# Performance work log

Measured on AMD Instinct MI355X. Metric: run time of the kernel, lower is better.

## Reference

```python
import jax, jax.numpy as jnp
import numpy as np

TOPK_FRAC = 0.9
LEAKY_SLOPE = 0.01
BN_EPS = 1e-5


def setup_inputs() -> dict:
    key = jax.random.key(0)
    k1, k2 = jax.random.split(key)
    B, C_in, N, C_out = 8, 256, 2048, 256
    x = jax.random.normal(k1, (B, C_in, N), dtype=jnp.float32)
    stdv = 1.0 / np.sqrt(C_out)
    weight = jax.random.uniform(k2, (C_in, C_out), dtype=jnp.float32, minval=-stdv, maxval=stdv)
    bn_weight = jnp.zeros((C_out,), dtype=jnp.float32)
    bn_bias = jnp.zeros((C_out,), dtype=jnp.float32)
    return {"x": x, "weight": weight, "bn_weight": bn_weight, "bn_bias": bn_bias}


def _norm_adj(xn):
    # xn: [B, N, C]
    adj = jax.nn.softmax(jnp.einsum('bnc,bmc->bnm', xn, xn), axis=-1)  # [B,N,N]
    N = adj.shape[1]
    k = int(round(N * TOPK_FRAC))
    topv, _ = jax.lax.top_k(adj, k)                     # [B,N,k]
    thresh = topv[..., -1:]                              # k-th largest per row
    return jnp.where(adj >= thresh, adj, 0.0)           # keep top-k, zero rest


def reference(x, weight, bn_weight, bn_bias):
    # x: [B, C_in, N] -> [B, N, C_in]
    xn = jnp.transpose(x, (0, 2, 1))
    adj = _norm_adj(xn)                                  # [B,N,N]
    support = jnp.einsum('bnc,cd->bnd', xn, weight)      # [B,N,C_out]
    out = jnp.einsum('bnm,bmd->bnd', adj, support)       # [B,N,C_out]
    out = jnp.transpose(out, (0, 2, 1))                  # [B,C_out,N]
    out = jnp.where(out >= 0, out, LEAKY_SLOPE * out)    # LeakyReLU
    # BatchNorm1d (training-mode batch stats) over (B, N) per channel
    mean = jnp.mean(out, axis=(0, 2), keepdims=True)
    var = jnp.mean(jnp.square(out - mean), axis=(0, 2), keepdims=True)
    out = (out - mean) * jax.lax.rsqrt(var + BN_EPS)
    return out * bn_weight[None, :, None] + bn_bias[None, :, None]
```

## Files before the change

kernel.cpp:

```cpp
#include <hip/hip_runtime.h>

#define B_ 8
#define C_ 256
#define N_ 2048
#define D_ 256
#define KKEEP 1843
#define LEAKY 0.01f
#define EPS 1e-5f

using short8  = __attribute__((ext_vector_type(8))) short;
using ushort8 = __attribute__((ext_vector_type(8))) unsigned short;
using ushort4v = __attribute__((ext_vector_type(4))) unsigned short;
using f32x4   = __attribute__((ext_vector_type(4))) float;

__device__ inline unsigned short f2bf(float x) {
  unsigned u = __float_as_uint(x);
  u += 0x7fffu + ((u >> 16) & 1u);
  return (unsigned short)(u >> 16);
}
__device__ inline float bf2f(unsigned short u) { return __uint_as_float(((unsigned)u) << 16); }

__device__ inline void gload16(const void* g, void* l) {
  __builtin_amdgcn_global_load_lds(
      (const __attribute__((address_space(1))) void*)g,
      (__attribute__((address_space(3))) void*)l, 16, 0, 0);
}

__global__ __launch_bounds__(256) void k_transpose_cast(const float* __restrict__ src,
                                                        unsigned short* __restrict__ dst,
                                                        int rows, int cols,
                                                        size_t srcBatch, size_t dstBatch) {
  __shared__ float tile[32][33];
  int b = blockIdx.z;
  src += (size_t)b * srcBatch;
  dst += (size_t)b * dstBatch;
  int i0 = blockIdx.y * 32;
  int j0 = blockIdx.x * 32;
  int t = threadIdx.x;
  int tc = t & 31, tr = t >> 5;
#pragma unroll
  for (int k = 0; k < 4; ++k)
    tile[tr + k * 8][tc] = src[(size_t)(i0 + tr + k * 8) * cols + j0 + tc];
  __syncthreads();
  int r2 = t >> 3, q = t & 7;
  ushort4v v;
#pragma unroll
  for (int l = 0; l < 4; ++l) v[l] = f2bf(tile[q * 4 + l][r2]);
  *(ushort4v*)&dst[(size_t)(j0 + r2) * rows + i0 + q * 4] = v;
}

template<int K_, int NX>
__global__ __launch_bounds__(256) void k_gemm(const short* __restrict__ A,
                                              const short* __restrict__ Bt,
                                              unsigned short* __restrict__ Cout,
                                              size_t aStride, size_t bStride, size_t cStride,
                                              int ldc) {
  __shared__ short As[128][64];
  __shared__ short Bs[128][64];
  int lin = blockIdx.x;
  int b = lin & 7;
  int rest = lin >> 3;
  int bxi = rest % NX, byi = rest / NX;
  const short* Ab = A + (size_t)b * aStride;
  const short* Bb = Bt + (size_t)b * bStride;
  int bi = byi * 128, bj = bxi * 128;
  int t = threadIdx.x, lane = t & 63, wid = t >> 6;
  int wr = (wid >> 1) * 64, wc = (wid & 1) * 64;
  int fr = lane & 15;
  int wbase = wid * 512;

  f32x4 acc[4][4];
  f32x4 z = {0.f, 0.f, 0.f, 0.f};
#pragma unroll
  for (int i = 0; i < 4; ++i)
#pragma unroll
    for (int j = 0; j < 4; ++j) acc[i][j] = z;

  for (int c0 = 0; c0 < K_; c0 += 64) {
    if (c0) __syncthreads();
#pragma unroll
    for (int i = 0; i < 4; ++i) {
      int li = i * 256 + t;
      int row = li >> 3, ch = li & 7;
      int sw = ((ch ^ (row & 7)) << 3);
      gload16(Ab + (size_t)(bi + row) * K_ + c0 + sw, (short*)As + i * 2048 + wbase);
      gload16(Bb + (size_t)(bj + row) * K_ + c0 + sw, (short*)Bs + i * 2048 + wbase);
    }
    __syncthreads();
#pragma unroll
    for (int ksub = 0; ksub < 2; ++ksub) {
      int cA = ksub * 4 + (lane >> 4);
      short8 af[4], bf[4];
#pragma unroll
      for (int f = 0; f < 4; ++f) {
        int R = wr + f * 16 + fr;
        af[f] = *(const short8*)&As[R][(cA ^ (R & 7)) << 3];
        int Rb = wc + f * 16 + fr;
        bf[f] = *(const short8*)&Bs[Rb][(cA ^ (Rb & 7)) << 3];
      }
#pragma unroll
      for (int fi = 0; fi < 4; ++fi)
#pragma unroll
        for (int fj = 0; fj < 4; ++fj)
          acc[fi][fj] = __builtin_amdgcn_mfma_f32_16x16x32_bf16(af[fi], bf[fj], acc[fi][fj], 0, 0, 0);
    }
  }

  int orow = (lane >> 4) * 4;
  int ocol = lane & 15;
#pragma unroll
  for (int fi = 0; fi < 4; ++fi)
#pragma unroll
    for (int fj = 0; fj < 4; ++fj)
#pragma unroll
      for (int r = 0; r < 4; ++r) {
        size_t idx = (size_t)b * cStride +
                     (size_t)(bi + wr + fi * 16 + orow + r) * ldc +
                     (size_t)(bj + wc + fj * 16 + ocol);
        Cout[idx] = f2bf(acc[fi][fj][r]);
      }
}

__global__ __launch_bounds__(256) void k_softmax_topk(unsigned short* __restrict__ S) {
  int t = threadIdx.x;
  int lane = t & 63, wv = t >> 6;
  size_t row = (size_t)blockIdx.x * 4 + wv;
  unsigned short* sr = S + row * N_;

  float e[32];
#pragma unroll
  for (int i = 0; i < 4; ++i) {
    ushort8 raw = *(const ushort8*)(sr + ((size_t)(i * 64 + lane)) * 8);
#pragma unroll
    for (int j = 0; j < 8; ++j) e[i * 8 + j] = bf2f(raw[j]);
  }

  float lm = e[0];
#pragma unroll
  for (int j = 1; j < 32; ++j) lm = fmaxf(lm, e[j]);
#pragma unroll
  for (int m = 1; m <= 16; m <<= 1) lm = fmaxf(lm, __shfl_xor(lm, m));
  lm = fmaxf(__shfl(lm, 0), __shfl(lm, 32));

  float ls = 0.f;
#pragma unroll
  for (int j = 0; j < 32; ++j) { e[j] = __expf(e[j] - lm); ls += e[j]; }
#pragma unroll
  for (int m = 1; m <= 16; m <<= 1) ls += __shfl_xor(ls, m);
  ls = __shfl(ls, 0) + __shfl(ls, 32);
  float inv = 1.0f / ls;

  unsigned kp[16], vo[16];
#pragma unroll
  for (int q = 0; q < 16; ++q)
    kp[q] = (unsigned)f2bf(e[q]) | ((unsigned)f2bf(e[q + 16]) << 16);
#pragma unroll
  for (int q = 0; q < 16; ++q)
    vo[q] = (unsigned)f2bf(e[2 * q] * inv) | ((unsigned)f2bf(e[2 * q + 1] * inv) << 16);

  unsigned tp[16];
#pragma unroll
  for (int q = 0; q < 16; ++q) tp[q] = kp[q];
#pragma unroll
  for (int sI = 0; sI < 4; ++sI) {
    const int s = 8 >> sI;
    const unsigned msk = (s == 8) ? 0x00FF00FFu : (s == 4) ? 0x0F0F0F0Fu
                       : (s == 2) ? 0x33333333u : 0x55555555u;
#pragma unroll
    for (int k = 0; k < 16; ++k) {
      if ((k & s) == 0) {
        unsigned tt = ((tp[k] >> s) ^ tp[k + s]) & msk;
        tp[k + s] ^= tt;
        tp[k]     ^= tt << s;
      }
    }
  }

  unsigned alive = 0xFFFFFFFFu, prefix = 0u;
  int need = KKEEP;
#pragma unroll
  for (int b = 12; b >= 0; b -= 2) {
    unsigned p1 = tp[b + 1], p0 = tp[b];
    unsigned hi = alive & p1;
    unsigned m3 = hi & p0, m2 = hi & ~p0, m1v = (alive & ~p1) & p0;
    unsigned packed = (unsigned)__popc(m3) | ((unsigned)__popc(m2) << 11) |
                      ((unsigned)__popc(m1v) << 22);
#pragma unroll
    for (int m = 1; m <= 16; m <<= 1) packed += __shfl_xor(packed, m);
    unsigned v0 = __shfl(packed, 0), v32 = __shfl(packed, 32);
    int C3 = (int)((v0 & 0x7FFu) + (v32 & 0x7FFu));
    int C2 = (int)(((v0 >> 11) & 0x7FFu) + ((v32 >> 11) & 0x7FFu));
    int C1 = (int)(((v0 >> 22) & 0x7FFu) + ((v32 >> 22) & 0x7FFu));
    int cum2 = C3 + C2, cum1 = cum2 + C1;
    if (C3 >= need)        { alive = m3;  prefix |= 3u << b; }
    else if (cum2 >= need) { alive = m2;  prefix |= 2u << b; need -= C3; }
    else if (cum1 >= need) { alive = m1v; prefix |= 1u << b; need -= cum2; }
    else                   { alive ^= (m3 | m2 | m1v);       need -= cum1; }
  }

#pragma unroll
  for (int i = 0; i < 4; ++i) {
    ushort8 o;
#pragma unroll
    for (int j = 0; j < 8; ++j) {
      int idx = i * 8 + j;
      unsigned key = (kp[idx & 15] >> ((idx >> 4) * 16)) & 0xFFFFu;
      unsigned val = (vo[idx >> 1] >> ((idx & 1) * 16)) & 0xFFFFu;
      o[j] = (key >= prefix) ? (unsigned short)val : (unsigned short)0;
    }
    *(ushort8*)(sr + ((size_t)(i * 64 + lane)) * 8) = o;
  }
}

__global__ __launch_bounds__(256) void k_pv(const short* __restrict__ A,
                                            const short* __restrict__ Bt,
                                            unsigned short* __restrict__ pre,
                                            float* __restrict__ ps, float* __restrict__ pss) {
  __shared__ short As[128][64];
  __shared__ short Bs[64][64];
  int lin = blockIdx.x;
  int b = lin & 7;
  int rest = lin >> 3;
  int bxi = rest & 3;
  int byi = rest >> 2;
  const short* Ab = A + (size_t)b * N_ * N_;
  const short* Bb = Bt + (size_t)b * D_ * N_;
  int bi = byi * 128, bj = bxi * 64;
  int t = threadIdx.x, lane = t & 63, wid = t >> 6;
  int wr = wid * 32;
  int fr = lane & 15;
  int wbase = wid * 512;

  f32x4 acc[2][4];
  f32x4 z = {0.f, 0.f, 0.f, 0.f};
#pragma unroll
  for (int i = 0; i < 2; ++i)
#pragma unroll
    for (int j = 0; j < 4; ++j) acc[i][j] = z;

  for (int c0 = 0; c0 < N_; c0 += 64) {
    if (c0) __syncthreads();
#pragma unroll
    for (int i = 0; i < 4; ++i) {
      int li = i * 256 + t;
      int row = li >> 3, ch = li & 7;
      int sw = ((ch ^ (row & 7)) << 3);
      gload16(Ab + (size_t)(bi + row) * N_ + c0 + sw, (short*)As + i * 2048 + wbase);
      if (i < 2)
        gload16(Bb + (size_t)(bj + row) * N_ + c0 + sw, (short*)Bs + i * 2048 + wbase);
    }
    __syncthreads();
#pragma unroll
    for (int ksub = 0; ksub < 2; ++ksub) {
      int cA = ksub * 4 + (lane >> 4);
      short8 af[2], bf[4];
#pragma unroll
      for (int f = 0; f < 2; ++f) {
        int R = wr + f * 16 + fr;
        af[f] = *(const short8*)&As[R][(cA ^ (R & 7)) << 3];
      }
#pragma unroll
      for (int f = 0; f < 4; ++f) {
        int Rb = f * 16 + fr;
        bf[f] = *(const short8*)&Bs[Rb][(cA ^ (Rb & 7)) << 3];
      }
#pragma unroll
      for (int fi = 0; fi < 2; ++fi)
#pragma unroll
        for (int fj = 0; fj < 4; ++fj)
          acc[fi][fj] = __builtin_amdgcn_mfma_f32_16x16x32_bf16(af[fi], bf[fj], acc[fi][fj], 0, 0, 0);
    }
  }

  int orow = (lane >> 4) * 4;
  int ocol = lane & 15;
  float s4[4] = {0.f, 0.f, 0.f, 0.f}, ss4[4] = {0.f, 0.f, 0.f, 0.f};
#pragma unroll
  for (int fi = 0; fi < 2; ++fi)
#pragma unroll
    for (int rr = 0; rr < 4; ++rr) {
      int rowg = bi + wr + fi * 16 + orow + rr;
      size_t base = ((size_t)b * N_ + rowg) * D_ + bj;
#pragma unroll
      for (int fj = 0; fj < 4; ++fj) {
        float v = acc[fi][fj][rr];
        v = (v >= 0.f) ? v : LEAKY * v;
        pre[base + fj * 16 + ocol] = f2bf(v);
        s4[fj] += v;
        ss4[fj] = fmaf(v, v, ss4[fj]);
      }
    }
#pragma unroll
  for (int fj = 0; fj < 4; ++fj) {
    s4[fj] += __shfl_xor(s4[fj], 16);  s4[fj] += __shfl_xor(s4[fj], 32);
    ss4[fj] += __shfl_xor(ss4[fj], 16); ss4[fj] += __shfl_xor(ss4[fj], 32);
  }
  __syncthreads();
  float* sred = (float*)As;
  if (lane < 16) {
#pragma unroll
    for (int fj = 0; fj < 4; ++fj) {
      sred[(wid * 4 + fj) * 16 + lane] = s4[fj];
      sred[256 + (wid * 4 + fj) * 16 + lane] = ss4[fj];
    }
  }
  __syncthreads();
  if (t < 64) {
    float s = 0.f, ss = 0.f;
#pragma unroll
    for (int w4 = 0; w4 < 4; ++w4) {
      s  += sred[(w4 * 4 + (t >> 4)) * 16 + (t & 15)];
      ss += sred[256 + (w4 * 4 + (t >> 4)) * 16 + (t & 15)];
    }
    ps[(size_t)lin * 64 + t] = s;
    pss[(size_t)lin * 64 + t] = ss;
  }
}

__global__ void k_final(const float* __restrict__ ps, const float* __restrict__ pss,
                        const float* __restrict__ bnw, const float* __restrict__ bnb,
                        float* __restrict__ scale, float* __restrict__ shift) {
  int t = threadIdx.x;
  int bxi = t >> 6, col = t & 63;
  float s = 0.f, ss = 0.f;
  for (int byi = 0; byi < 16; ++byi)
    for (int bb = 0; bb < 8; ++bb) {
      int lin = (byi * 4 + bxi) * 8 + bb;
      s += ps[(size_t)lin * 64 + col];
      ss += pss[(size_t)lin * 64 + col];
    }
  const float invN = 1.0f / (B_ * N_);
  float mean = s * invN;
  float var = fmaf(-mean, mean, ss * invN);
  float istd = rsqrtf(var + EPS);
  float sc = istd * bnw[t];
  scale[t] = sc;
  shift[t] = fmaf(-mean, sc, bnb[t]);
}

__global__ __launch_bounds__(256) void k_out(const unsigned short* __restrict__ pre,
                                             const float* __restrict__ scale,
                                             const float* __restrict__ shift,
                                             float* __restrict__ out) {
  __shared__ float tile[32][33];
  int blk = blockIdx.x;
  int d0 = (blk % (D_ / 32)) * 32;
  int n0 = ((blk / (D_ / 32)) % (N_ / 32)) * 32;
  int b = blk / ((D_ / 32) * (N_ / 32));
  int tc = threadIdx.x & 31;
  int tr = threadIdx.x >> 5;
  const unsigned short* pb = pre + ((size_t)b * N_ + n0) * D_ + d0;
#pragma unroll
  for (int i = 0; i < 4; ++i) {
    int r = tr + i * 8;
    tile[r][tc] = bf2f(pb[(size_t)r * D_ + tc]);
  }
  __syncthreads();
  float* ob = out + ((size_t)b * D_ + d0) * N_ + n0;
#pragma unroll
  for (int i = 0; i < 4; ++i) {
    int r = tr + i * 8;
    float vv = tile[tc][r];
    ob[(size_t)r * N_ + tc] = fmaf(vv, scale[d0 + r], shift[d0 + r]);
  }
}

extern "C" void kernel_launch(void* const* d_in, const int* in_sizes, int n_in,
                              void* d_out, int out_size, void* d_ws, size_t ws_size,
                              hipStream_t stream) {
  const float* x = (const float*)d_in[0];
  const float* W = (const float*)d_in[1];
  const float* bnw = (const float*)d_in[2];
  const float* bnb = (const float*)d_in[3];
  float* out = (float*)d_out;

  char* w = (char*)d_ws;
  short* xt = (short*)w;            w += (size_t)B_ * N_ * C_ * 2;
  short* wt = (short*)w;            w += (size_t)D_ * C_ * 2;
  short* supT = (short*)w;          w += (size_t)B_ * D_ * N_ * 2;
  short* S = (short*)w;             w += (size_t)B_ * N_ * N_ * 2;
  unsigned short* pre = (unsigned short*)w; w += (size_t)B_ * N_ * D_ * 2;
  float* ps = (float*)w;            w += (size_t)512 * 64 * 4;
  float* pss = (float*)w;           w += (size_t)512 * 64 * 4;
  float* scale = (float*)w;         w += D_ * 4;
  float* shift = (float*)w;         w += D_ * 4;

  k_transpose_cast<<<dim3(N_ / 32, C_ / 32, B_), 256, 0, stream>>>(
      x, (unsigned short*)xt, C_, N_, (size_t)C_ * N_, (size_t)N_ * C_);
  k_transpose_cast<<<dim3(D_ / 32, C_ / 32, 1), 256, 0, stream>>>(
      W, (unsigned short*)wt, C_, D_, 0, 0);

  k_gemm<C_, 16><<<dim3(8 * 16 * 2, 1, 1), 256, 0, stream>>>(
      wt, xt, (unsigned short*)supT, 0, (size_t)N_ * C_, (size_t)D_ * N_, N_);

  k_gemm<C_, 16><<<dim3(8 * 16 * 16, 1, 1), 256, 0, stream>>>(
      xt, xt, (unsigned short*)S, (size_t)N_ * C_, (size_t)N_ * C_, (size_t)N_ * N_, N_);

  k_softmax_topk<<<B_ * N_ / 4, 256, 0, stream>>>((unsigned short*)S);

  k_pv<<<dim3(4 * 16 * 8, 1, 1), 256, 0, stream>>>(S, supT, pre, ps, pss);

  k_final<<<1, 256, 0, stream>>>(ps, pss, bnw, bnb, scale, shift);
  k_out<<<B_ * (N_ / 32) * (D_ / 32), 256, 0, stream>>>(pre, scale, shift, out);
}
```

Measured before the change: 108.4 us.

## Interleave batches across blocks for XCD locality and split PV tile over 8 waves

Block indices in transpose, softmax-topk and output kernels are remapped so the batch index is the low bits. This likely keeps each batch's data on one XCD's L2 on the MI355X. The PV GEMM now runs 512 threads with a 4x2 wave grid, each wave computing 32x32 instead of 32x64, to raise wave-level parallelism per tile. The final BN reduction is split across 4 blocks. The trade-off is that each wave does fewer MFMAs per LDS load and the block uses more registers.

```diff
diff --git a/kernel.cpp b/kernel.cpp
--- a/kernel.cpp
+++ b/kernel.cpp
@@ -26,16 +26,24 @@
       (__attribute__((address_space(3))) void*)l, 16, 0, 0);
 }
 
+template<bool PIN>
 __global__ __launch_bounds__(256) void k_transpose_cast(const float* __restrict__ src,
                                                         unsigned short* __restrict__ dst,
-                                                        int rows, int cols,
+                                                        int rows, int cols, int njt,
                                                         size_t srcBatch, size_t dstBatch) {
   __shared__ float tile[32][33];
-  int b = blockIdx.z;
+  int b, i0, j0;
+  if constexpr (PIN) {
+    int lin = blockIdx.x;
+    b = lin & 7;
+    int rest = lin >> 3;
+    j0 = (rest % njt) * 32;
+    i0 = (rest / njt) * 32;
+  } else {
+    b = blockIdx.z; j0 = blockIdx.x * 32; i0 = blockIdx.y * 32;
+  }
   src += (size_t)b * srcBatch;
   dst += (size_t)b * dstBatch;
-  int i0 = blockIdx.y * 32;
-  int j0 = blockIdx.x * 32;
   int t = threadIdx.x;
   int tc = t & 31, tr = t >> 5;
 #pragma unroll
@@ -124,7 +132,10 @@
 __global__ __launch_bounds__(256) void k_softmax_topk(unsigned short* __restrict__ S) {
   int t = threadIdx.x;
   int lane = t & 63, wv = t >> 6;
-  size_t row = (size_t)blockIdx.x * 4 + wv;
+  int lin = blockIdx.x;
+  int b = lin & 7;
+  int grp = lin >> 3;
+  size_t row = (size_t)b * N_ + grp * 4 + wv;
   unsigned short* sr = S + row * N_;
 
   float e[32];
@@ -179,8 +190,8 @@
   unsigned alive = 0xFFFFFFFFu, prefix = 0u;
   int need = KKEEP;
 #pragma unroll
-  for (int b = 12; b >= 0; b -= 2) {
-    unsigned p1 = tp[b + 1], p0 = tp[b];
+  for (int b2 = 12; b2 >= 0; b2 -= 2) {
+    unsigned p1 = tp[b2 + 1], p0 = tp[b2];
     unsigned hi = alive & p1;
     unsigned m3 = hi & p0, m2 = hi & ~p0, m1v = (alive & ~p1) & p0;
     unsigned packed = (unsigned)__popc(m3) | ((unsigned)__popc(m2) << 11) |
@@ -192,10 +203,10 @@
     int C2 = (int)(((v0 >> 11) & 0x7FFu) + ((v32 >> 11) & 0x7FFu));
     int C1 = (int)(((v0 >> 22) & 0x7FFu) + ((v32 >> 22) & 0x7FFu));
     int cum2 = C3 + C2, cum1 = cum2 + C1;
-    if (C3 >= need)        { alive = m3;  prefix |= 3u << b; }
-    else if (cum2 >= need) { alive = m2;  prefix |= 2u << b; need -= C3; }
-    else if (cum1 >= need) { alive = m1v; prefix |= 1u << b; need -= cum2; }
-    else                   { alive ^= (m3 | m2 | m1v);       need -= cum1; }
+    if (C3 >= need)        { alive = m3;  prefix |= 3u << b2; }
+    else if (cum2 >= need) { alive = m2;  prefix |= 2u << b2; need -= C3; }
+    else if (cum1 >= need) { alive = m1v; prefix |= 1u << b2; need -= cum2; }
+    else                   { alive ^= (m3 | m2 | m1v);        need -= cum1; }
   }
 
 #pragma unroll
@@ -212,7 +223,7 @@
   }
 }
 
-__global__ __launch_bounds__(256) void k_pv(const short* __restrict__ A,
+__global__ __launch_bounds__(512) void k_pv(const short* __restrict__ A,
                                             const short* __restrict__ Bt,
                                             unsigned short* __restrict__ pre,
                                             float* __restrict__ ps, float* __restrict__ pss) {
@@ -226,55 +237,52 @@
   const short* Ab = A + (size_t)b * N_ * N_;
   const short* Bb = Bt + (size_t)b * D_ * N_;
   int bi = byi * 128, bj = bxi * 64;
-  int t = threadIdx.x, lane = t & 63, wid = t >> 6;
-  int wr = wid * 32;
+  int t = threadIdx.x, lane = t & 63, w = t >> 6;
+  int wr = (w >> 1) * 32, wc = (w & 1) * 32;
   int fr = lane & 15;
-  int wbase = wid * 512;
-
-  f32x4 acc[2][4];
+
+  f32x4 acc[2][2];
   f32x4 z = {0.f, 0.f, 0.f, 0.f};
 #pragma unroll
   for (int i = 0; i < 2; ++i)
 #pragma unroll
-    for (int j = 0; j < 4; ++j) acc[i][j] = z;
+    for (int j = 0; j < 2; ++j) acc[i][j] = z;
 
   for (int c0 = 0; c0 < N_; c0 += 64) {
     if (c0) __syncthreads();
-#pragma unroll
-    for (int i = 0; i < 4; ++i) {
-      int li = i * 256 + t;
-      int row = li >> 3, ch = li & 7;
+    {
+      int row = t >> 3, ch = t & 7;
       int sw = ((ch ^ (row & 7)) << 3);
-      gload16(Ab + (size_t)(bi + row) * N_ + c0 + sw, (short*)As + i * 2048 + wbase);
-      if (i < 2)
-        gload16(Bb + (size_t)(bj + row) * N_ + c0 + sw, (short*)Bs + i * 2048 + wbase);
+      gload16(Ab + (size_t)(bi + row) * N_ + c0 + sw, (short*)As + w * 512);
+      gload16(Bb + (size_t)(bj + row) * N_ + c0 + sw, (short*)Bs + w * 512);
+      int li = 512 + t;
+      int row1 = li >> 3, ch1 = li & 7;
+      int sw1 = ((ch1 ^ (row1 & 7)) << 3);
+      gload16(Ab + (size_t)(bi + row1) * N_ + c0 + sw1, (short*)As + 4096 + w * 512);
     }
     __syncthreads();
 #pragma unroll
     for (int ksub = 0; ksub < 2; ++ksub) {
       int cA = ksub * 4 + (lane >> 4);
-      short8 af[2], bf[4];
+      short8 af[2], bf[2];
 #pragma unroll
       for (int f = 0; f < 2; ++f) {
         int R = wr + f * 16 + fr;
         af[f] = *(const short8*)&As[R][(cA ^ (R & 7)) << 3];
-      }
-#pragma unroll
-      for (int f = 0; f < 4; ++f) {
-        int Rb = f * 16 + fr;
+        int Rb = wc + f * 16 + fr;
         bf[f] = *(const short8*)&Bs[Rb][(cA ^ (Rb & 7)) << 3];
       }
 #pragma unroll
       for (int fi = 0; fi < 2; ++fi)
 #pragma unroll
-        for (int fj = 0; fj < 4; ++fj)
+        for (int fj = 0; fj < 2; ++fj)
           acc[fi][fj] = __builtin_amdgcn_mfma_f32_16x16x32_bf16(af[fi], bf[fj], acc[fi][fj], 0, 0, 0);
     }
   }
 
   int orow = (lane >> 4) * 4;
   int ocol = lane & 15;
-  float s4[4] = {0.f, 0.f, 0.f, 0.f}, ss4[4] = {0.f, 0.f, 0.f, 0.f};
+  float s2[2] = {0.f, 0.f}, ss2[2] = {0.f, 0.f};
 #pragma unroll
   for (int fi = 0; fi < 2; ++fi)
 #pragma unroll
@@ -282,35 +290,37 @@
       int rowg = bi + wr + fi * 16 + orow + rr;
       size_t base = ((size_t)b * N_ + rowg) * D_ + bj;
 #pragma unroll
-      for (int fj = 0; fj < 4; ++fj) {
+      for (int fj = 0; fj < 2; ++fj) {
         float v = acc[fi][fj][rr];
         v = (v >= 0.f) ? v : LEAKY * v;
-        pre[base + fj * 16 + ocol] = f2bf(v);
-        s4[fj] += v;
-        ss4[fj] = fmaf(v, v, ss4[fj]);
+        pre[base + wc + fj * 16 + ocol] = f2bf(v);
+        s2[fj] += v;
+        ss2[fj] = fmaf(v, v, ss2[fj]);
       }
     }
 #pragma unroll
-  for (int fj = 0; fj < 4; ++fj) {
-    s4[fj] += __shfl_xor(s4[fj], 16);  s4[fj] += __shfl_xor(s4[fj], 32);
-    ss4[fj] += __shfl_xor(ss4[fj], 16); ss4[fj] += __shfl_xor(ss4[fj], 32);
+  for (int fj = 0; fj < 2; ++fj) {
+    s2[fj] += __shfl_xor(s2[fj], 16);  s2[fj] += __shfl_xor(s2[fj], 32);
+    ss2[fj] += __shfl_xor(ss2[fj], 16); ss2[fj] += __shfl_xor(ss2[fj], 32);
   }
   __syncthreads();
   float* sred = (float*)As;
   if (lane < 16) {
 #pragma unroll
-    for (int fj = 0; fj < 4; ++fj) {
-      sred[(wid * 4 + fj) * 16 + lane] = s4[fj];
-      sred[256 + (wid * 4 + fj) * 16 + lane] = ss4[fj];
+    for (int fj = 0; fj < 2; ++fj) {
+      sred[(w * 2 + fj) * 16 + lane] = s2[fj];
+      sred[256 + (w * 2 + fj) * 16 + lane] = ss2[fj];
     }
   }
   __syncthreads();
   if (t < 64) {
+    int cw = t >> 5, fj = (t >> 4) & 1, oc = t & 15;
     float s = 0.f, ss = 0.f;
 #pragma unroll
-    for (int w4 = 0; w4 < 4; ++w4) {
-      s  += sred[(w4 * 4 + (t >> 4)) * 16 + (t & 15)];
-      ss += sred[256 + (w4 * 4 + (t >> 4)) * 16 + (t & 15)];
+    for (int rw = 0; rw < 4; ++rw) {
+      int w2 = rw * 2 + cw;
+      s  += sred[(w2 * 2 + fj) * 16 + oc];
+      ss += sred[256 + (w2 * 2 + fj) * 16 + oc];
     }
     ps[(size_t)lin * 64 + t] = s;
     pss[(size_t)lin * 64 + t] = ss;
@@ -320,8 +330,9 @@
 __global__ void k_final(const float* __restrict__ ps, const float* __restrict__ pss,
                         const float* __restrict__ bnw, const float* __restrict__ bnb,
                         float* __restrict__ scale, float* __restrict__ shift) {
-  int t = threadIdx.x;
-  int bxi = t >> 6, col = t & 63;
+  int col = threadIdx.x;
+  int bxi = blockIdx.x;
+  int ch = bxi * 64 + col;
   float s = 0.f, ss = 0.f;
   for (int byi = 0; byi < 16; ++byi)
     for (int bb = 0; bb < 8; ++bb) {
@@ -333,9 +344,9 @@
   float mean = s * invN;
   float var = fmaf(-mean, mean, ss * invN);
   float istd = rsqrtf(var + EPS);
-  float sc = istd * bnw[t];
-  scale[t] = sc;
-  shift[t] = fmaf(-mean, sc, bnb[t]);
+  float sc = istd * bnw[ch];
+  scale[ch] = sc;
+  shift[ch] = fmaf(-mean, sc, bnb[ch]);
 }
 
 __global__ __launch_bounds__(256) void k_out(const unsigned short* __restrict__ pre,
@@ -343,10 +354,11 @@
                                              const float* __restrict__ shift,
                                              float* __restrict__ out) {
   __shared__ float tile[32][33];
-  int blk = blockIdx.x;
-  int d0 = (blk % (D_ / 32)) * 32;
-  int n0 = ((blk / (D_ / 32)) % (N_ / 32)) * 32;
-  int b = blk / ((D_ / 32) * (N_ / 32));
+  int lin = blockIdx.x;
+  int b = lin & 7;
+  int rest = lin >> 3;
+  int d0 = (rest & 7) * 32;
+  int n0 = (rest >> 3) * 32;
   int tc = threadIdx.x & 31;
   int tr = threadIdx.x >> 5;
   const unsigned short* pb = pre + ((size_t)b * N_ + n0) * D_ + d0;
@@ -385,10 +397,10 @@
   float* scale = (float*)w;         w += D_ * 4;
   float* shift = (float*)w;         w += D_ * 4;
 
-  k_transpose_cast<<<dim3(N_ / 32, C_ / 32, B_), 256, 0, stream>>>(
-      x, (unsigned short*)xt, C_, N_, (size_t)C_ * N_, (size_t)N_ * C_);
-  k_transpose_cast<<<dim3(D_ / 32, C_ / 32, 1), 256, 0, stream>>>(
-      W, (unsigned short*)wt, C_, D_, 0, 0);
+  k_transpose_cast<true><<<dim3(8 * 64 * 8, 1, 1), 256, 0, stream>>>(
+      x, (unsigned short*)xt, C_, N_, 64, (size_t)C_ * N_, (size_t)N_ * C_);
+  k_transpose_cast<false><<<dim3(D_ / 32, C_ / 32, 1), 256, 0, stream>>>(
+      W, (unsigned short*)wt, C_, D_, 0, 0, 0);
 
   k_gemm<C_, 16><<<dim3(8 * 16 * 2, 1, 1), 256, 0, stream>>>(
       wt, xt, (unsigned short*)supT, 0, (size_t)N_ * C_, (size_t)D_ * N_, N_);
@@ -398,8 +410,8 @@
 
   k_softmax_topk<<<B_ * N_ / 4, 256, 0, stream>>>((unsigned short*)S);
 
-  k_pv<<<dim3(4 * 16 * 8, 1, 1), 256, 0, stream>>>(S, supT, pre, ps, pss);
-
-  k_final<<<1, 256, 0, stream>>>(ps, pss, bnw, bnb, scale, shift);
+  k_pv<<<dim3(4 * 16 * 8, 1, 1), 512, 0, stream>>>(S, supT, pre, ps, pss);
+
+  k_final<<<4, 64, 0, stream>>>(ps, pss, bnw, bnb, scale, shift);
   k_out<<<B_ * (N_ / 32) * (D_ / 32), 256, 0, stream>>>(pre, scale, shift, out);
 }
```

Result: no change. 109.4 us (+0.9%).

## Exploit Gram symmetry for xx^T and remap block indices batch-innermost

Applied to the files above, without the earlier changes.

Replaces the general GEMM that computes the per-batch similarity matrix with a symmetric Gram kernel. It launches only the upper-triangular 128x128 tiles and writes each off-diagonal tile a second time, transposed through LDS, to fill the mirror block. This roughly halves the MFMA work for that matrix, at the cost of an extra LDS transpose and a second store per off-diagonal tile. Several other kernels (transpose-cast, softmax/top-k, output) now put the batch index in the low bits of the block index so neighbouring blocks work on different batches, and the BN final reduction is split over four blocks.

```diff
diff --git a/kernel.cpp b/kernel.cpp
--- a/kernel.cpp
+++ b/kernel.cpp
@@ -26,16 +26,24 @@
       (__attribute__((address_space(3))) void*)l, 16, 0, 0);
 }
 
+template<bool PIN>
 __global__ __launch_bounds__(256) void k_transpose_cast(const float* __restrict__ src,
                                                         unsigned short* __restrict__ dst,
-                                                        int rows, int cols,
+                                                        int rows, int cols, int njt,
                                                         size_t srcBatch, size_t dstBatch) {
   __shared__ float tile[32][33];
-  int b = blockIdx.z;
+  int b, i0, j0;
+  if constexpr (PIN) {
+    int lin = blockIdx.x;
+    b = lin & 7;
+    int rest = lin >> 3;
+    j0 = (rest % njt) * 32;
+    i0 = (rest / njt) * 32;
+  } else {
+    b = blockIdx.z; j0 = blockIdx.x * 32; i0 = blockIdx.y * 32;
+  }
   src += (size_t)b * srcBatch;
   dst += (size_t)b * dstBatch;
-  int i0 = blockIdx.y * 32;
-  int j0 = blockIdx.x * 32;
   int t = threadIdx.x;
   int tc = t & 31, tr = t >> 5;
 #pragma unroll
@@ -121,10 +129,107 @@
       }
 }
 
+__global__ __launch_bounds__(256) void k_gram(const short* __restrict__ A,
+                                              unsigned short* __restrict__ Cout,
+                                              size_t aStride, size_t cStride, int ldc) {
+  __shared__ short lds[16896];
+  short (*As)[64] = (short(*)[64])lds;
+  short (*Bs)[64] = (short(*)[64])(lds + 8192);
+  int lin = blockIdx.x;
+  int b = lin & 7;
+  int rest = lin >> 3;
+  int byi = 0;
+  while (rest >= 16 - byi) { rest -= 16 - byi; ++byi; }
+  int bxi = byi + rest;
+  const short* Ab = A + (size_t)b * aStride;
+  int bi = byi * 128, bj = bxi * 128;
+  int t = threadIdx.x, lane = t & 63, wid = t >> 6;
+  int wr = (wid >> 1) * 64, wc = (wid & 1) * 64;
+  int fr = lane & 15;
+  int wbase = wid * 512;
+
+  f32x4 acc[4][4];
+  f32x4 z = {0.f, 0.f, 0.f, 0.f};
+#pragma unroll
+  for (int i = 0; i < 4; ++i)
+#pragma unroll
+    for (int j = 0; j < 4; ++j) acc[i][j] = z;
+
+  for (int c0 = 0; c0 < C_; c0 += 64) {
+    if (c0) __syncthreads();
+#pragma unroll
+    for (int i = 0; i < 4; ++i) {
+      int li = i * 256 + t;
+      int row = li >> 3, ch = li & 7;
+      int sw = ((ch ^ (row & 7)) << 3);
+      gload16(Ab + (size_t)(bi + row) * C_ + c0 + sw, lds + i * 2048 + wbase);
+      gload16(Ab + (size_t)(bj + row) * C_ + c0 + sw, lds + 8192 + i * 2048 + wbase);
+    }
+    __syncthreads();
+#pragma unroll
+    for (int ksub = 0; ksub < 2; ++ksub) {
+      int cA = ksub * 4 + (lane >> 4);
+      short8 af[4], bf[4];
+#pragma unroll
+      for (int f = 0; f < 4; ++f) {
+        int R = wr + f * 16 + fr;
+        af[f] = *(const short8*)&As[R][(cA ^ (R & 7)) << 3];
+        int Rb = wc + f * 16 + fr;
+        bf[f] = *(const short8*)&Bs[Rb][(cA ^ (Rb & 7)) << 3];
+      }
+#pragma unroll
+      for (int fi = 0; fi < 4; ++fi)
+#pragma unroll
+        for (int fj = 0; fj < 4; ++fj)
+          acc[fi][fj] = __builtin_amdgcn_mfma_f32_16x16x32_bf16(af[fi], bf[fj], acc[fi][fj], 0, 0, 0);
+    }
+  }
+
+  int orow = (lane >> 4) * 4;
+  int ocol = lane & 15;
+  unsigned short* Sb = Cout + (size_t)b * cStride;
+
+#pragma unroll
+  for (int fi = 0; fi < 4; ++fi)
+#pragma unroll
+    for (int fj = 0; fj < 4; ++fj)
+#pragma unroll
+      for (int r = 0; r < 4; ++r)
+        Sb[(size_t)(bi + wr + fi * 16 + orow + r) * ldc +
+           (bj + wc + fj * 16 + ocol)] = f2bf(acc[fi][fj][r]);
+
+  if (bxi != byi) {
+    __syncthreads();
+    short* ep = lds;
+#pragma unroll
+    for (int fi = 0; fi < 4; ++fi)
+#pragma unroll
+      for (int fj = 0; fj < 4; ++fj) {
+        int col = wc + fj * 16 + ocol;
+        int row0 = wr + fi * 16 + orow;
+        unsigned lo = (unsigned)f2bf(acc[fi][fj][0]) | ((unsigned)f2bf(acc[fi][fj][1]) << 16);
+        unsigned hi = (unsigned)f2bf(acc[fi][fj][2]) | ((unsigned)f2bf(acc[fi][fj][3]) << 16);
+        unsigned* p = (unsigned*)&ep[col * 132 + row0];
+        p[0] = lo; p[1] = hi;
+      }
+    __syncthreads();
+#pragma unroll
+    for (int i2 = 0; i2 < 8; ++i2) {
+      int id = i2 * 256 + t;
+      int oc = id >> 4, q = id & 15;
+      ushort8 v8 = *(const ushort8*)&ep[oc * 132 + q * 8];
+      *(ushort8*)&Sb[(size_t)(bj + oc) * ldc + bi + q * 8] = v8;
+    }
+  }
+}
+
 __global__ __launch_bounds__(256) void k_softmax_topk(unsigned short* __restrict__ S) {
   int t = threadIdx.x;
   int lane = t & 63, wv = t >> 6;
-  size_t row = (size_t)blockIdx.x * 4 + wv;
+  int lin = blockIdx.x;
+  int b = lin & 7;
+  int grp = lin >> 3;
+  size_t row = (size_t)b * N_ + grp * 4 + wv;
   unsigned short* sr = S + row * N_;
 
   float e[32];
@@ -179,8 +284,8 @@
   unsigned alive = 0xFFFFFFFFu, prefix = 0u;
   int need = KKEEP;
 #pragma unroll
-  for (int b = 12; b >= 0; b -= 2) {
-    unsigned p1 = tp[b + 1], p0 = tp[b];
+  for (int b2 = 12; b2 >= 0; b2 -= 2) {
+    unsigned p1 = tp[b2 + 1], p0 = tp[b2];
     unsigned hi = alive & p1;
     unsigned m3 = hi & p0, m2 = hi & ~p0, m1v = (alive & ~p1) & p0;
     unsigned packed = (unsigned)__popc(m3) | ((unsigned)__popc(m2) << 11) |
@@ -192,10 +297,10 @@
     int C2 = (int)(((v0 >> 11) & 0x7FFu) + ((v32 >> 11) & 0x7FFu));
     int C1 = (int)(((v0 >> 22) & 0x7FFu) + ((v32 >> 22) & 0x7FFu));
     int cum2 = C3 + C2, cum1 = cum2 + C1;
-    if (C3 >= need)        { alive = m3;  prefix |= 3u << b; }
-    else if (cum2 >= need) { alive = m2;  prefix |= 2u << b; need -= C3; }
-    else if (cum1 >= need) { alive = m1v; prefix |= 1u << b; need -= cum2; }
-    else                   { alive ^= (m3 | m2 | m1v);       need -= cum1; }
+    if (C3 >= need)        { alive = m3;  prefix |= 3u << b2; }
+    else if (cum2 >= need) { alive = m2;  prefix |= 2u << b2; need -= C3; }
+    else if (cum1 >= need) { alive = m1v; prefix |= 1u << b2; need -= cum2; }
+    else                   { alive ^= (m3 | m2 | m1v);        need -= cum1; }
   }
 
 #pragma unroll
@@ -320,8 +425,9 @@
 __global__ void k_final(const float* __restrict__ ps, const float* __restrict__ pss,
                         const float* __restrict__ bnw, const float* __restrict__ bnb,
                         float* __restrict__ scale, float* __restrict__ shift) {
-  int t = threadIdx.x;
-  int bxi = t >> 6, col = t & 63;
+  int col = threadIdx.x;
+  int bxi = blockIdx.x;
+  int ch = bxi * 64 + col;
   float s = 0.f, ss = 0.f;
   for (int byi = 0; byi < 16; ++byi)
     for (int bb = 0; bb < 8; ++bb) {
@@ -333,9 +439,9 @@
   float mean = s * invN;
   float var = fmaf(-mean, mean, ss * invN);
   float istd = rsqrtf(var + EPS);
-  float sc = istd * bnw[t];
-  scale[t] = sc;
-  shift[t] = fmaf(-mean, sc, bnb[t]);
+  float sc = istd * bnw[ch];
+  scale[ch] = sc;
+  shift[ch] = fmaf(-mean, sc, bnb[ch]);
 }
 
 __global__ __launch_bounds__(256) void k_out(const unsigned short* __restrict__ pre,
@@ -343,10 +449,11 @@
                                              const float* __restrict__ shift,
                                              float* __restrict__ out) {
   __shared__ float tile[32][33];
-  int blk = blockIdx.x;
-  int d0 = (blk % (D_ / 32)) * 32;
-  int n0 = ((blk / (D_ / 32)) % (N_ / 32)) * 32;
-  int b = blk / ((D_ / 32) * (N_ / 32));
+  int lin = blockIdx.x;
+  int b = lin & 7;
+  int rest = lin >> 3;
+  int d0 = (rest & 7) * 32;
+  int n0 = (rest >> 3) * 32;
   int tc = threadIdx.x & 31;
   int tr = threadIdx.x >> 5;
   const unsigned short* pb = pre + ((size_t)b * N_ + n0) * D_ + d0;
@@ -385,21 +492,21 @@
   float* scale = (float*)w;         w += D_ * 4;
   float* shift = (float*)w;         w += D_ * 4;
 
-  k_transpose_cast<<<dim3(N_ / 32, C_ / 32, B_), 256, 0, stream>>>(
-      x, (unsigned short*)xt, C_, N_, (size_t)C_ * N_, (size_t)N_ * C_);
-  k_transpose_cast<<<dim3(D_ / 32, C_ / 32, 1), 256, 0, stream>>>(
-      W, (unsigned short*)wt, C_, D_, 0, 0);
+  k_transpose_cast<true><<<dim3(8 * 64 * 8, 1, 1), 256, 0, stream>>>(
+      x, (unsigned short*)xt, C_, N_, 64, (size_t)C_ * N_, (size_t)N_ * C_);
+  k_transpose_cast<false><<<dim3(D_ / 32, C_ / 32, 1), 256, 0, stream>>>(
+      W, (unsigned short*)wt, C_, D_, 0, 0, 0);
 
   k_gemm<C_, 16><<<dim3(8 * 16 * 2, 1, 1), 256, 0, stream>>>(
       wt, xt, (unsigned short*)supT, 0, (size_t)N_ * C_, (size_t)D_ * N_, N_);
 
-  k_gemm<C_, 16><<<dim3(8 * 16 * 16, 1, 1), 256, 0, stream>>>(
-      xt, xt, (unsigned short*)S, (size_t)N_ * C_, (size_t)N_ * C_, (size_t)N_ * N_, N_);
+  k_gram<<<dim3(8 * 136, 1, 1), 256, 0, stream>>>(
+      xt, (unsigned short*)S, (size_t)N_ * C_, (size_t)N_ * N_, N_);
 
   k_softmax_topk<<<B_ * N_ / 4, 256, 0, stream>>>((unsigned short*)S);
 
   k_pv<<<dim3(4 * 16 * 8, 1, 1), 256, 0, stream>>>(S, supT, pre, ps, pss);
 
-  k_final<<<1, 256, 0, stream>>>(ps, pss, bnw, bnb, scale, shift);
+  k_final<<<4, 64, 0, stream>>>(ps, pss, bnw, bnb, scale, shift);
   k_out<<<B_ * (N_ / 32) * (D_ / 32), 256, 0, stream>>>(pre, scale, shift, out);
 }
```

New measurement: 107.9 us. Within noise of the previous version (-0.5%).
